# Kernel optimization log

Measured on AMD Instinct MI355X. Metric: run time of the kernel, lower is better.

## Reference

```python
import jax, jax.numpy as jnp
import numpy as np

N = 50000        # nodes
E = 1600000      # edges (avg degree 32)
INDIM = 256
OUTDIM = 64
HEADS = 4


def setup_inputs() -> dict:
    key = jax.random.key(0)
    k = jax.random.split(key, 7)
    h = jax.random.normal(k[0], (N, INDIM), dtype=jnp.float32)
    e = jax.random.normal(k[1], (E, 1), dtype=jnp.float32)
    norm = jax.random.uniform(k[2], (N, 1), dtype=jnp.float32)
    src = jax.random.randint(k[3], (E,), 0, N)
    dst = jax.random.randint(k[4], (E,), 0, N)
    # per-head params: W: Linear(indim->outdim, bias=False); a: Linear(2*outdim->1, bias=False)
    W = jax.random.normal(k[5], (HEADS, INDIM, OUTDIM), dtype=jnp.float32) * 0.05
    a = jax.random.normal(k[6], (HEADS, 2 * OUTDIM), dtype=jnp.float32) * 0.05
    return {"h": h, "e": e, "norm": norm, "src": src, "dst": dst, "W": W, "a": a}


def reference(h, e, norm, src, dst, W, a):
    n = h.shape[0]
    h_in = h
    hs = h * norm                      # [N, indim]
    head_outs = []
    for i in range(HEADS):             # small fixed head count
        z = hs @ W[i]                  # [N, outdim]
        # attn score: a^T [z_src ; z_dst] decomposed into per-node halves
        s_src = z @ a[i, :OUTDIM]      # [N]
        s_dst = z @ a[i, OUTDIM:]      # [N]
        score = s_src[src] + s_dst[dst]                      # [E]
        # segment softmax over incoming edges of each dst node
        m = jax.ops.segment_max(score, dst, num_segments=n)  # [N]
        m = jnp.where(jnp.isfinite(m), m, 0.0)
        ex = jnp.exp(score - m[dst])                         # [E]
        den = jax.ops.segment_sum(ex, dst, num_segments=n)   # [N]
        alpha = ex / den[dst]                                # [E]
        # scatter-weighted sum of source features
        hh = jax.ops.segment_sum(alpha[:, None] * z[src], dst, num_segments=n)  # [N, outdim]
        head_outs.append(hh * norm)
    hout = jnp.concatenate(head_outs, axis=1)   # [N, outdim*heads] == [N, indim]
    return (h_in + hout, e)
```

## Files before the change

### kernel.cpp

```cpp
#include <hip/hip_runtime.h>

#define NN 50000
#define NE 1600000
#define IND 256
#define OUTD 64
#define NH 4
#define EPB 4096
#define NBLKP 391
#define NBUCK 196

typedef __attribute__((ext_vector_type(8))) short short8;
typedef __attribute__((ext_vector_type(4))) float f32x4;

__device__ __forceinline__ unsigned short f2bf(float x) {
    unsigned int u = __float_as_uint(x);
    u = (u + 0x7FFFu + ((u >> 16) & 1u)) >> 16;
    return (unsigned short)u;
}
__device__ __forceinline__ float bf2f(unsigned short u) {
    return __uint_as_float((unsigned int)u << 16);
}

__global__ __launch_bounds__(256) void k_wt(const float* __restrict__ W, unsigned short* __restrict__ Wt,
                                            const float4* __restrict__ e4, float4* __restrict__ oute4) {
    int t = blockIdx.x * 256 + threadIdx.x;
    int c = t >> 8, k = t & 255;
    Wt[t] = f2bf(W[(c >> 6) * IND * OUTD + k * OUTD + (c & 63)]);
    for (int i = t; i < NE / 4; i += 65536) oute4[i] = e4[i];
}

__global__ __launch_bounds__(256) void k_gmm(const float* __restrict__ h, const float* __restrict__ norm,
                                             const unsigned short* __restrict__ Wt, const float* __restrict__ a,
                                             unsigned short* __restrict__ zb,
                                             float* __restrict__ ssrc, float* __restrict__ sdst) {
    __shared__ unsigned short lds[4][16 * 80];
    const int lane = threadIdx.x & 63;
    const int wv = threadIdx.x >> 6;
    const int m0 = blockIdx.x * 64;
    const int c0 = wv * 64;
    const int r16 = lane & 15, kg = lane >> 4;

    float nm[4];
    const float4* hp[4];
    #pragma unroll
    for (int mt = 0; mt < 4; ++mt) {
        int rr = m0 + mt * 16 + r16; if (rr > NN - 1) rr = NN - 1;
        nm[mt] = norm[rr];
        hp[mt] = (const float4*)(h + (size_t)rr * IND + kg * 8);
    }
    const short8* bp[4];
    #pragma unroll
    for (int nt = 0; nt < 4; ++nt)
        bp[nt] = (const short8*)(Wt + (size_t)(c0 + nt * 16 + r16) * IND + kg * 8);

    f32x4 acc[4][4] = {};

    float4 xA[4], xB[4];
    short8 bb[4];
    #pragma unroll
    for (int mt = 0; mt < 4; ++mt) { xA[mt] = hp[mt][0]; xB[mt] = hp[mt][1]; }
    #pragma unroll
    for (int nt = 0; nt < 4; ++nt) bb[nt] = bp[nt][0];

    #pragma unroll
    for (int ks = 0; ks < 8; ++ks) {
        short8 av[4], cb[4];
        #pragma unroll
        for (int mt = 0; mt < 4; ++mt) {
            av[mt][0] = (short)f2bf(xA[mt].x * nm[mt]);
            av[mt][1] = (short)f2bf(xA[mt].y * nm[mt]);
            av[mt][2] = (short)f2bf(xA[mt].z * nm[mt]);
            av[mt][3] = (short)f2bf(xA[mt].w * nm[mt]);
            av[mt][4] = (short)f2bf(xB[mt].x * nm[mt]);
            av[mt][5] = (short)f2bf(xB[mt].y * nm[mt]);
            av[mt][6] = (short)f2bf(xB[mt].z * nm[mt]);
            av[mt][7] = (short)f2bf(xB[mt].w * nm[mt]);
        }
        #pragma unroll
        for (int nt = 0; nt < 4; ++nt) cb[nt] = bb[nt];
        if (ks < 7) {
            #pragma unroll
            for (int mt = 0; mt < 4; ++mt) {
                xA[mt] = hp[mt][(ks + 1) * 8];
                xB[mt] = hp[mt][(ks + 1) * 8 + 1];
            }
            #pragma unroll
            for (int nt = 0; nt < 4; ++nt) bb[nt] = bp[nt][(ks + 1) * 4];
        }
        #pragma unroll
        for (int mt = 0; mt < 4; ++mt) {
            #pragma unroll
            for (int nt = 0; nt < 4; ++nt)
                acc[mt][nt] = __builtin_amdgcn_mfma_f32_16x16x32_bf16(av[mt], cb[nt], acc[mt][nt], 0, 0, 0);
        }
    }

    float asrc[4], adst[4];
    #pragma unroll
    for (int j = 0; j < 4; ++j) {
        asrc[j] = a[wv * 128 + j * 16 + r16];
        adst[j] = a[wv * 128 + 64 + j * 16 + r16];
    }
    #pragma unroll
    for (int mt = 0; mt < 4; ++mt) {
        #pragma unroll
        for (int r = 0; r < 4; ++r) {
            int row = m0 + mt * 16 + kg * 4 + r;
            unsigned short q0 = f2bf(acc[mt][0][r]);
            unsigned short q1 = f2bf(acc[mt][1][r]);
            unsigned short q2 = f2bf(acc[mt][2][r]);
            unsigned short q3 = f2bf(acc[mt][3][r]);
            float ps = bf2f(q0) * asrc[0] + bf2f(q1) * asrc[1] + bf2f(q2) * asrc[2] + bf2f(q3) * asrc[3];
            float pd = bf2f(q0) * adst[0] + bf2f(q1) * adst[1] + bf2f(q2) * adst[2] + bf2f(q3) * adst[3];
            #pragma unroll
            for (int off = 1; off < 16; off <<= 1) {
                ps += __shfl_xor(ps, off);
                pd += __shfl_xor(pd, off);
            }
            unsigned short* lp = &lds[wv][(kg * 4 + r) * 80];
            lp[ 0 + r16] = q0;
            lp[16 + r16] = q1;
            lp[32 + r16] = q2;
            lp[48 + r16] = q3;
            if (row < NN && r16 == 0) {
                ssrc[(row << 2) + wv] = ps;
                sdst[(row << 2) + wv] = pd;
            }
        }
        asm volatile("s_waitcnt lgkmcnt(0)" ::: "memory");
        __builtin_amdgcn_sched_barrier(0);
        #pragma unroll
        for (int hf = 0; hf < 2; ++hf) {
            int lrow = hf * 8 + (lane >> 3);
            int chunk = lane & 7;
            short8 v = *(const short8*)&lds[wv][lrow * 80 + chunk * 8];
            int grow = m0 + mt * 16 + lrow;
            if (grow < NN)
                *(short8*)(zb + (size_t)grow * IND + c0 + chunk * 8) = v;
        }
        __builtin_amdgcn_sched_barrier(0);
    }
}

__global__ __launch_bounds__(256) void k_phist(const int* __restrict__ dst, int* __restrict__ bh) {
    __shared__ int lh[NBUCK];
    int tid = threadIdx.x;
    if (tid < NBUCK) lh[tid] = 0;
    __syncthreads();
    int base = blockIdx.x * EPB;
    for (int i = tid; i < EPB; i += 256) {
        int ed = base + i;
        if (ed < NE) atomicAdd(&lh[dst[ed] >> 8], 1);
    }
    __syncthreads();
    if (tid < NBUCK) bh[blockIdx.x * NBUCK + tid] = lh[tid];
}

__global__ __launch_bounds__(256) void k_poffA(const int* __restrict__ bh, int* __restrict__ goff,
                                               int* __restrict__ colsum) {
    __shared__ int wsum[4];
    int t = blockIdx.x;
    int tid = threadIdx.x;
    int b0 = tid * 2, b1 = tid * 2 + 1;
    int v0 = (b0 < NBLKP) ? bh[b0 * NBUCK + t] : 0;
    int v1 = (b1 < NBLKP) ? bh[b1 * NBUCK + t] : 0;
    int s = v0 + v1;
    int lane = tid & 63, w = tid >> 6;
    int x = s;
    #pragma unroll
    for (int off = 1; off < 64; off <<= 1) {
        int tmp = __shfl_up(x, off);
        if (lane >= off) x += tmp;
    }
    if (lane == 63) wsum[w] = x;
    __syncthreads();
    int waveoff = 0;
    for (int j = 0; j < w; ++j) waveoff += wsum[j];
    int excl = waveoff + x - s;
    if (b0 < NBLKP) goff[b0 * NBUCK + t] = excl;
    if (b1 < NBLKP) goff[b1 * NBUCK + t] = excl + v0;
    if (tid == 255) colsum[t] = waveoff + x;
}

__global__ __launch_bounds__(256) void k_poffB(const int* __restrict__ colsum, int* __restrict__ bstart) {
    __shared__ int wsum[4];
    int tid = threadIdx.x;
    int v = (tid < NBUCK) ? colsum[tid] : 0;
    int lane = tid & 63, w = tid >> 6;
    int x = v;
    #pragma unroll
    for (int off = 1; off < 64; off <<= 1) {
        int tmp = __shfl_up(x, off);
        if (lane >= off) x += tmp;
    }
    if (lane == 63) wsum[w] = x;
    __syncthreads();
    int waveoff = 0;
    for (int j = 0; j < w; ++j) waveoff += wsum[j];
    if (tid < NBUCK) bstart[tid] = waveoff + x - v;
    if (tid == 0) bstart[NBUCK] = NE;
}

__global__ __launch_bounds__(256) void k_pscat(const int* __restrict__ src, const int* __restrict__ dst,
                                               const int* __restrict__ goff, const int* __restrict__ bstart,
                                               unsigned int* __restrict__ tmp) {
    __shared__ int lcur[NBUCK];
    __shared__ int bs[NBUCK];
    int tid = threadIdx.x;
    if (tid < NBUCK) { lcur[tid] = 0; bs[tid] = bstart[tid]; }
    __syncthreads();
    int base = blockIdx.x * EPB;
    const int* go = goff + blockIdx.x * NBUCK;
    for (int i = tid; i < EPB; i += 256) {
        int ed = base + i;
        if (ed < NE) {
            int d = dst[ed];
            int bin = d >> 8;
            int r = atomicAdd(&lcur[bin], 1);
            tmp[bs[bin] + go[bin] + r] = ((unsigned int)(d & 255) << 16) | (unsigned int)src[ed];
        }
    }
}

__global__ __launch_bounds__(256) void k_lsort(const unsigned int* __restrict__ tmp,
                                               const int* __restrict__ bstart,
                                               int* __restrict__ rowp, int* __restrict__ srcs) {
    __shared__ int lh[256], lcur[256], wsum[4];
    int b = blockIdx.x, tid = threadIdx.x;
    int base = bstart[b], cnt = bstart[b + 1] - base;
    lh[tid] = 0;
    __syncthreads();
    for (int i = tid; i < cnt; i += 256) {
        int dloc = (int)(tmp[base + i] >> 16) & 255;
        atomicAdd(&lh[dloc], 1);
    }
    __syncthreads();
    int lane = tid & 63, w = tid >> 6;
    int v = lh[tid];
    int x = v;
    #pragma unroll
    for (int off = 1; off < 64; off <<= 1) {
        int t2 = __shfl_up(x, off);
        if (lane >= off) x += t2;
    }
    if (lane == 63) wsum[w] = x;
    __syncthreads();
    int waveoff = 0;
    for (int j = 0; j < w; ++j) waveoff += wsum[j];
    int excl = waveoff + x - v;
    lcur[tid] = excl;
    int d = (b << 8) + tid;
    if (d < NN) rowp[d] = base + excl;
    if (b == NBUCK - 1 && tid == 0) rowp[NN] = NE;
    __syncthreads();
    for (int i = tid; i < cnt; i += 256) {
        unsigned int rec = tmp[base + i];
        int dloc = (int)(rec >> 16) & 255;
        int p = atomicAdd(&lcur[dloc], 1);
        srcs[base + p] = (int)(rec & 0xFFFFu);
    }
}

__global__ __launch_bounds__(256) void k_agg(const unsigned short* __restrict__ zb, const int* __restrict__ rowp,
                                             const int* __restrict__ srcs, const float* __restrict__ ssrc,
                                             const float* __restrict__ sdst,
                                             const float* __restrict__ h, const float* __restrict__ norm,
                                             float* __restrict__ out) {
    int wv = threadIdx.x >> 6, lane = threadIdx.x & 63;
    int half = lane >> 5;
    int l = lane & 31;
    int n = blockIdx.x * 8 + wv * 2 + half;
    if (n >= NN) return;
    int p0 = rowp[n], p1 = rowp[n + 1];
    int deg = p1 - p0;
    int hd = l >> 3;
    float sd = sdst[(n << 2) + hd];
    float a0 = 0.f, a1 = 0.f, a2 = 0.f, a3 = 0.f;
    float a4 = 0.f, a5 = 0.f, a6 = 0.f, a7 = 0.f;
    float b0 = 0.f, b1 = 0.f, b2 = 0.f, b3 = 0.f;
    float b4 = 0.f, b5 = 0.f, b6 = 0.f, b7 = 0.f;
    float denA = 0.f, denB = 0.f;
    int zoffl = l << 3;
    int i = 0;
    for (; i + 4 <= deg; i += 4) {
        int s0 = srcs[p0 + i];
        int s1 = srcs[p0 + i + 1];
        int s2 = srcs[p0 + i + 2];
        int s3 = srcs[p0 + i + 3];
        float w0 = __expf(ssrc[(s0 << 2) + hd] + sd);
        float w1 = __expf(ssrc[(s1 << 2) + hd] + sd);
        float w2 = __expf(ssrc[(s2 << 2) + hd] + sd);
        float w3 = __expf(ssrc[(s3 << 2) + hd] + sd);
        uint4 z0 = *(const uint4*)(zb + (s0 << 8) + zoffl);
        uint4 z1 = *(const uint4*)(zb + (s1 << 8) + zoffl);
        uint4 z2 = *(const uint4*)(zb + (s2 << 8) + zoffl);
        uint4 z3 = *(const uint4*)(zb + (s3 << 8) + zoffl);
        a0 += w0 * bf2f((unsigned short)(z0.x & 0xFFFFu));
        a1 += w0 * bf2f((unsigned short)(z0.x >> 16));
        a2 += w0 * bf2f((unsigned short)(z0.y & 0xFFFFu));
        a3 += w0 * bf2f((unsigned short)(z0.y >> 16));
        a4 += w0 * bf2f((unsigned short)(z0.z & 0xFFFFu));
        a5 += w0 * bf2f((unsigned short)(z0.z >> 16));
        a6 += w0 * bf2f((unsigned short)(z0.w & 0xFFFFu));
        a7 += w0 * bf2f((unsigned short)(z0.w >> 16));
        denA += w0;
        b0 += w1 * bf2f((unsigned short)(z1.x & 0xFFFFu));
        b1 += w1 * bf2f((unsigned short)(z1.x >> 16));
        b2 += w1 * bf2f((unsigned short)(z1.y & 0xFFFFu));
        b3 += w1 * bf2f((unsigned short)(z1.y >> 16));
        b4 += w1 * bf2f((unsigned short)(z1.z & 0xFFFFu));
        b5 += w1 * bf2f((unsigned short)(z1.z >> 16));
        b6 += w1 * bf2f((unsigned short)(z1.w & 0xFFFFu));
        b7 += w1 * bf2f((unsigned short)(z1.w >> 16));
        denB += w1;
        a0 += w2 * bf2f((unsigned short)(z2.x & 0xFFFFu));
        a1 += w2 * bf2f((unsigned short)(z2.x >> 16));
        a2 += w2 * bf2f((unsigned short)(z2.y & 0xFFFFu));
        a3 += w2 * bf2f((unsigned short)(z2.y >> 16));
        a4 += w2 * bf2f((unsigned short)(z2.z & 0xFFFFu));
        a5 += w2 * bf2f((unsigned short)(z2.z >> 16));
        a6 += w2 * bf2f((unsigned short)(z2.w & 0xFFFFu));
        a7 += w2 * bf2f((unsigned short)(z2.w >> 16));
        denA += w2;
        b0 += w3 * bf2f((unsigned short)(z3.x & 0xFFFFu));
        b1 += w3 * bf2f((unsigned short)(z3.x >> 16));
        b2 += w3 * bf2f((unsigned short)(z3.y & 0xFFFFu));
        b3 += w3 * bf2f((unsigned short)(z3.y >> 16));
        b4 += w3 * bf2f((unsigned short)(z3.z & 0xFFFFu));
        b5 += w3 * bf2f((unsigned short)(z3.z >> 16));
        b6 += w3 * bf2f((unsigned short)(z3.w & 0xFFFFu));
        b7 += w3 * bf2f((unsigned short)(z3.w >> 16));
        denB += w3;
    }
    for (; i < deg; ++i) {
        int s0 = srcs[p0 + i];
        float w0 = __expf(ssrc[(s0 << 2) + hd] + sd);
        uint4 z0 = *(const uint4*)(zb + (s0 << 8) + zoffl);
        a0 += w0 * bf2f((unsigned short)(z0.x & 0xFFFFu));
        a1 += w0 * bf2f((unsigned short)(z0.x >> 16));
        a2 += w0 * bf2f((unsigned short)(z0.y & 0xFFFFu));
        a3 += w0 * bf2f((unsigned short)(z0.y >> 16));
        a4 += w0 * bf2f((unsigned short)(z0.z & 0xFFFFu));
        a5 += w0 * bf2f((unsigned short)(z0.z >> 16));
        a6 += w0 * bf2f((unsigned short)(z0.w & 0xFFFFu));
        a7 += w0 * bf2f((unsigned short)(z0.w >> 16));
        denA += w0;
    }
    a0 += b0; a1 += b1; a2 += b2; a3 += b3;
    a4 += b4; a5 += b5; a6 += b6; a7 += b7;
    float den = denA + denB;
    float nm = norm[n];
    float inv = (deg > 0) ? nm / den : 0.f;
    size_t bofs = (size_t)n * IND + zoffl;
    float4 h0 = *(const float4*)(h + bofs);
    float4 h1 = *(const float4*)(h + bofs + 4);
    float4 o0, o1;
    o0.x = h0.x + inv * a0; o0.y = h0.y + inv * a1;
    o0.z = h0.z + inv * a2; o0.w = h0.w + inv * a3;
    o1.x = h1.x + inv * a4; o1.y = h1.y + inv * a5;
    o1.z = h1.z + inv * a6; o1.w = h1.w + inv * a7;
    *(float4*)(out + bofs) = o0;
    *(float4*)(out + bofs + 4) = o1;
}

extern "C" void kernel_launch(void* const* d_in, const int* in_sizes, int n_in,
                              void* d_out, int out_size, void* d_ws, size_t ws_size,
                              hipStream_t stream) {
    const float* h    = (const float*)d_in[0];
    const float* e    = (const float*)d_in[1];
    const float* norm = (const float*)d_in[2];
    const int*   src  = (const int*)d_in[3];
    const int*   dst  = (const int*)d_in[4];
    const float* W    = (const float*)d_in[5];
    const float* a    = (const float*)d_in[6];
    float* out = (float*)d_out;

    char* p = (char*)d_ws;
    unsigned short* Wt = (unsigned short*)p; p += 262144;
    unsigned short* zb = (unsigned short*)p; p += 25600000;
    float* ssrc = (float*)p; p += 800000;
    float* sdst = (float*)p; p += 800000;
    int*   rowp = (int*)p;   p += 200192;
    int*   srcs = (int*)p;   p += 6400000;
    int*   bh   = (int*)p;   p += 307200;
    int*   goff = (int*)p;   p += 307200;
    int*   bstart = (int*)p; p += 4096;
    int*   colsum = (int*)p; p += 4096;
    unsigned int* tmp = (unsigned int*)p; p += 6400000;

    k_wt<<<256, 256, 0, stream>>>(W, Wt, (const float4*)e, (float4*)(out + (size_t)NN * IND));
    k_gmm<<<782, 256, 0, stream>>>(h, norm, Wt, a, zb, ssrc, sdst);
    k_phist<<<NBLKP, 256, 0, stream>>>(dst, bh);
    k_poffA<<<NBUCK, 256, 0, stream>>>(bh, goff, colsum);
    k_poffB<<<1, 256, 0, stream>>>(colsum, bstart);
    k_pscat<<<NBLKP, 256, 0, stream>>>(src, dst, goff, bstart, tmp);
    k_lsort<<<NBUCK, 256, 0, stream>>>(tmp, bstart, rowp, srcs);
    k_agg<<<6250, 256, 0, stream>>>(zb, rowp, srcs, ssrc, sdst, h, norm, out);
}
```

Before: 240.7 us.

## Stage scaled bf16 A tile in LDS and pre-swizzle W into MFMA fragment order

Before, each wave loaded and converted the same h rows itself, so every row was read and converted four times. Now the block cooperatively loads 32 rows of h, scales them by norm, converts them to bf16 once into a padded LDS tile, and every wave reads its A fragments from there. W is rearranged in the prep kernel into per-lane MFMA fragment order, giving contiguous, coalesced B loads. Rows per block drop from 64 to 32, doubling the grid. The cost is a __syncthreads, more LDS per block, and less register-level software prefetch of B.

```diff
diff --git a/kernel.cpp b/kernel.cpp
--- a/kernel.cpp
+++ b/kernel.cpp
@@ -21,77 +21,62 @@
     return __uint_as_float((unsigned int)u << 16);
 }
 
-__global__ __launch_bounds__(256) void k_wt(const float* __restrict__ W, unsigned short* __restrict__ Wt,
+__global__ __launch_bounds__(256) void k_wt(const float* __restrict__ W, unsigned short* __restrict__ Wtf,
                                             const float4* __restrict__ e4, float4* __restrict__ oute4) {
     int t = blockIdx.x * 256 + threadIdx.x;
-    int c = t >> 8, k = t & 255;
-    Wt[t] = f2bf(W[(c >> 6) * IND * OUTD + k * OUTD + (c & 63)]);
+    int e = t & 7;
+    int lane = (t >> 3) & 63;
+    int ks = (t >> 9) & 7;
+    int nt = (t >> 12) & 3;
+    int hd = (t >> 14) & 3;
+    int k = ks * 32 + (lane >> 4) * 8 + e;
+    int d = nt * 16 + (lane & 15);
+    Wtf[t] = f2bf(W[hd * IND * OUTD + k * OUTD + d]);
     for (int i = t; i < NE / 4; i += 65536) oute4[i] = e4[i];
 }
 
 __global__ __launch_bounds__(256) void k_gmm(const float* __restrict__ h, const float* __restrict__ norm,
-                                             const unsigned short* __restrict__ Wt, const float* __restrict__ a,
+                                             const unsigned short* __restrict__ Wtf, const float* __restrict__ a,
                                              unsigned short* __restrict__ zb,
                                              float* __restrict__ ssrc, float* __restrict__ sdst) {
-    __shared__ unsigned short lds[4][16 * 80];
-    const int lane = threadIdx.x & 63;
-    const int wv = threadIdx.x >> 6;
-    const int m0 = blockIdx.x * 64;
+    __shared__ unsigned short ldsA[32 * 264];
+    __shared__ unsigned short ldsE[4][16 * 80];
+    const int tid = threadIdx.x;
+    const int lane = tid & 63;
+    const int wv = tid >> 6;
+    const int m0 = blockIdx.x * 32;
     const int c0 = wv * 64;
     const int r16 = lane & 15, kg = lane >> 4;
 
-    float nm[4];
-    const float4* hp[4];
-    #pragma unroll
-    for (int mt = 0; mt < 4; ++mt) {
-        int rr = m0 + mt * 16 + r16; if (rr > NN - 1) rr = NN - 1;
-        nm[mt] = norm[rr];
-        hp[mt] = (const float4*)(h + (size_t)rr * IND + kg * 8);
-    }
-    const short8* bp[4];
-    #pragma unroll
-    for (int nt = 0; nt < 4; ++nt)
-        bp[nt] = (const short8*)(Wt + (size_t)(c0 + nt * 16 + r16) * IND + kg * 8);
-
-    f32x4 acc[4][4] = {};
-
-    float4 xA[4], xB[4];
-    short8 bb[4];
-    #pragma unroll
-    for (int mt = 0; mt < 4; ++mt) { xA[mt] = hp[mt][0]; xB[mt] = hp[mt][1]; }
-    #pragma unroll
-    for (int nt = 0; nt < 4; ++nt) bb[nt] = bp[nt][0];
-
+    #pragma unroll
+    for (int q = 0; q < 4; ++q) {
+        int idx = q * 2048 + tid * 8;
+        int row = idx >> 8, col = idx & 255;
+        int grow = m0 + row; if (grow > NN - 1) grow = NN - 1;
+        float nmv = norm[grow];
+        const float4* hp = (const float4*)(h + (size_t)grow * IND + col);
+        float4 x0 = hp[0], x1 = hp[1];
+        short8 r;
+        r[0] = (short)f2bf(x0.x * nmv); r[1] = (short)f2bf(x0.y * nmv);
+        r[2] = (short)f2bf(x0.z * nmv); r[3] = (short)f2bf(x0.w * nmv);
+        r[4] = (short)f2bf(x1.x * nmv); r[5] = (short)f2bf(x1.y * nmv);
+        r[6] = (short)f2bf(x1.z * nmv); r[7] = (short)f2bf(x1.w * nmv);
+        *(short8*)&ldsA[row * 264 + col] = r;
+    }
+    __syncthreads();
+
+    const short8* bfp = (const short8*)(Wtf) + (size_t)wv * 4 * 8 * 64;
+
+    f32x4 acc[2][4] = {};
     #pragma unroll
     for (int ks = 0; ks < 8; ++ks) {
-        short8 av[4], cb[4];
+        short8 av0 = *(const short8*)&ldsA[r16 * 264 + ks * 32 + kg * 8];
+        short8 av1 = *(const short8*)&ldsA[(16 + r16) * 264 + ks * 32 + kg * 8];
         #pragma unroll
-        for (int mt = 0; mt < 4; ++mt) {
-            av[mt][0] = (short)f2bf(xA[mt].x * nm[mt]);
-            av[mt][1] = (short)f2bf(xA[mt].y * nm[mt]);
-            av[mt][2] = (short)f2bf(xA[mt].z * nm[mt]);
-            av[mt][3] = (short)f2bf(xA[mt].w * nm[mt]);
-            av[mt][4] = (short)f2bf(xB[mt].x * nm[mt]);
-            av[mt][5] = (short)f2bf(xB[mt].y * nm[mt]);
-            av[mt][6] = (short)f2bf(xB[mt].z * nm[mt]);
-            av[mt][7] = (short)f2bf(xB[mt].w * nm[mt]);
-        }
-        #pragma unroll
-        for (int nt = 0; nt < 4; ++nt) cb[nt] = bb[nt];
-        if (ks < 7) {
-            #pragma unroll
-            for (int mt = 0; mt < 4; ++mt) {
-                xA[mt] = hp[mt][(ks + 1) * 8];
-                xB[mt] = hp[mt][(ks + 1) * 8 + 1];
-            }
-            #pragma unroll
-            for (int nt = 0; nt < 4; ++nt) bb[nt] = bp[nt][(ks + 1) * 4];
-        }
-        #pragma unroll
-        for (int mt = 0; mt < 4; ++mt) {
-            #pragma unroll
-            for (int nt = 0; nt < 4; ++nt)
-                acc[mt][nt] = __builtin_amdgcn_mfma_f32_16x16x32_bf16(av[mt], cb[nt], acc[mt][nt], 0, 0, 0);
+        for (int nt = 0; nt < 4; ++nt) {
+            short8 cb = bfp[(nt * 8 + ks) * 64 + lane];
+            acc[0][nt] = __builtin_amdgcn_mfma_f32_16x16x32_bf16(av0, cb, acc[0][nt], 0, 0, 0);
+            acc[1][nt] = __builtin_amdgcn_mfma_f32_16x16x32_bf16(av1, cb, acc[1][nt], 0, 0, 0);
         }
     }
 
@@ -102,7 +87,7 @@
         adst[j] = a[wv * 128 + 64 + j * 16 + r16];
     }
     #pragma unroll
-    for (int mt = 0; mt < 4; ++mt) {
+    for (int mt = 0; mt < 2; ++mt) {
         #pragma unroll
         for (int r = 0; r < 4; ++r) {
             int row = m0 + mt * 16 + kg * 4 + r;
@@ -117,7 +102,7 @@
                 ps += __shfl_xor(ps, off);
                 pd += __shfl_xor(pd, off);
             }
-            unsigned short* lp = &lds[wv][(kg * 4 + r) * 80];
+            unsigned short* lp = &ldsE[wv][(kg * 4 + r) * 80];
             lp[ 0 + r16] = q0;
             lp[16 + r16] = q1;
             lp[32 + r16] = q2;
@@ -133,7 +118,7 @@
         for (int hf = 0; hf < 2; ++hf) {
             int lrow = hf * 8 + (lane >> 3);
             int chunk = lane & 7;
-            short8 v = *(const short8*)&lds[wv][lrow * 80 + chunk * 8];
+            short8 v = *(const short8*)&ldsE[wv][lrow * 80 + chunk * 8];
             int grow = m0 + mt * 16 + lrow;
             if (grow < NN)
                 *(short8*)(zb + (size_t)grow * IND + c0 + chunk * 8) = v;
@@ -376,7 +361,7 @@
     float* out = (float*)d_out;
 
     char* p = (char*)d_ws;
-    unsigned short* Wt = (unsigned short*)p; p += 262144;
+    unsigned short* Wtf = (unsigned short*)p; p += 262144;
     unsigned short* zb = (unsigned short*)p; p += 25600000;
     float* ssrc = (float*)p; p += 800000;
     float* sdst = (float*)p; p += 800000;
@@ -388,8 +373,8 @@
     int*   colsum = (int*)p; p += 4096;
     unsigned int* tmp = (unsigned int*)p; p += 6400000;
 
-    k_wt<<<256, 256, 0, stream>>>(W, Wt, (const float4*)e, (float4*)(out + (size_t)NN * IND));
-    k_gmm<<<782, 256, 0, stream>>>(h, norm, Wt, a, zb, ssrc, sdst);
+    k_wt<<<256, 256, 0, stream>>>(W, Wtf, (const float4*)e, (float4*)(out + (size_t)NN * IND));
+    k_gmm<<<1563, 256, 0, stream>>>(h, norm, Wtf, a, zb, ssrc, sdst);
     k_phist<<<NBLKP, 256, 0, stream>>>(dst, bh);
     k_poffA<<<NBUCK, 256, 0, stream>>>(bh, goff, colsum);
     k_poffB<<<1, 256, 0, stream>>>(colsum, bstart);
```

Result: faster. 208.4 us (-13.4%).
